# Kernel optimization log

Hardware: AMD Instinct MI355X
Metric: run time of the kernel (lower is better)

The kernel has to match this reference:

```python
import jax, jax.numpy as jnp
import numpy as np

VOCAB = 1500   # vocab_size
NE = 208       # n_embed
T = 256        # block_size
NH = 4         # n_head
HD = NE // NH  # head_size = 52
NL = 8         # n_layer
B = 256        # batch


def setup_inputs() -> dict:
    key = jax.random.key(0)
    ks = jax.random.split(key, 16)
    f = lambda k, shape: jax.random.normal(k, shape, jnp.float32) * 0.02
    return {
        "idx": jax.random.randint(ks[0], (B, T), 0, VOCAB),
        "targets": jax.random.randint(ks[1], (B, T), 0, VOCAB),
        "tok_emb": f(ks[2], (VOCAB, NE)),
        "pos_emb": f(ks[3], (T, NE)),
        # per-layer stacked attention params (separate no-bias Q/K/V Linears per head)
        "Wq": f(ks[4], (NL, NH, NE, HD)),
        "Wk": f(ks[5], (NL, NH, NE, HD)),
        "Wv": f(ks[6], (NL, NH, NE, HD)),
        "Wo": f(ks[7], (NL, NE, NE)),
        "bo": jnp.zeros((NL, NE), jnp.float32),
        "ln1_g": jnp.ones((NL, NE), jnp.float32),
        "ln1_b": jnp.zeros((NL, NE), jnp.float32),
        "W1": f(ks[8], (NL, NE, 4 * NE)),
        "b1": jnp.zeros((NL, 4 * NE), jnp.float32),
        "W2": f(ks[9], (NL, 4 * NE, NE)),
        "b2": jnp.zeros((NL, NE), jnp.float32),
        "ln2_g": jnp.ones((NL, NE), jnp.float32),
        "ln2_b": jnp.zeros((NL, NE), jnp.float32),
        "lnf_g": jnp.ones((NE,), jnp.float32),
        "lnf_b": jnp.zeros((NE,), jnp.float32),
        "Wlm": f(ks[10], (NE, VOCAB)),
        "blm": jnp.zeros((VOCAB,), jnp.float32),
    }


def _layernorm(x, g, b, eps=1e-5):
    mu = x.mean(-1, keepdims=True)
    var = ((x - mu) ** 2).mean(-1, keepdims=True)
    return (x - mu) * jax.lax.rsqrt(var + eps) * g + b


def reference(idx, targets, tok_emb, pos_emb, Wq, Wk, Wv, Wo, bo,
              ln1_g, ln1_b, W1, b1, W2, b2, ln2_g, ln2_b,
              lnf_g, lnf_b, Wlm, blm):
    x = tok_emb[idx] + pos_emb[None, :, :]          # [B, T, NE]
    mask = jnp.tril(jnp.ones((T, T), bool))
    scale = NE ** -0.5                               # NOTE: scales by n_embed, per source (C**-0.5)
    for i in range(NL):
        h = _layernorm(x, ln1_g[i], ln1_b[i])
        q = jnp.einsum('btc,hcd->bhtd', h, Wq[i])
        k = jnp.einsum('btc,hcd->bhtd', h, Wk[i])
        v = jnp.einsum('btc,hcd->bhtd', h, Wv[i])
        s = jnp.einsum('bhtd,bhsd->bhts', q, k) * scale
        s = jnp.where(mask, s, -jnp.inf)
        a = jax.nn.softmax(s, axis=-1)               # dropout is identity in eval
        o = jnp.einsum('bhts,bhsd->bhtd', a, v)
        o = o.transpose(0, 2, 1, 3).reshape(x.shape[0], T, NE)
        x = x + o @ Wo[i] + bo[i]
        h2 = _layernorm(x, ln2_g[i], ln2_b[i])
        x = x + jax.nn.relu(h2 @ W1[i] + b1[i]) @ W2[i] + b2[i]
    x = _layernorm(x, lnf_g, lnf_b)
    logits = (x @ Wlm + blm).reshape(-1, VOCAB)      # [B*T, VOCAB]
    logp = jax.nn.log_softmax(logits, axis=-1)
    loss = -jnp.take_along_axis(logp, targets.reshape(-1, 1), axis=-1).mean()
    return logits, loss
```

## Files before the change

kernel.cpp:

```cpp
#include <hip/hip_runtime.h>
#include <hip/hip_bf16.h>
#include <math.h>

#define VOCAB 1500
#define NE    208
#define TT    256
#define NHD   4
#define HD    52
#define NL    8
#define BBATCH 256
#define NTOK  (BBATCH * TT)
#define KP    224

typedef __attribute__((ext_vector_type(8))) short bf16x8;
typedef __attribute__((ext_vector_type(4))) short s16x4;
typedef __attribute__((ext_vector_type(4))) float f32x4;
typedef __attribute__((ext_vector_type(4))) int i32x4;
typedef __attribute__((ext_vector_type(4))) _Float16 f16x4;

__device__ __forceinline__ void gload16(const void* g, void* l) {
  __builtin_amdgcn_global_load_lds(
      (const __attribute__((address_space(1))) unsigned int*)g,
      (__attribute__((address_space(3))) unsigned int*)l, 16, 0, 0);
}
__device__ __forceinline__ float bf2f(short u) {
  union { unsigned int i; float f; } cv;
  cv.i = ((unsigned int)(unsigned short)u) << 16;
  return cv.f;
}
__device__ __forceinline__ short f2bf(float f) {
  return (short)__bfloat16_as_ushort(__float2bfloat16(f));
}

#define P_QKV 1146880
#define P_O   458752
#define P_1   1605632
#define P_2   1703936
#define P_LM  344064
__global__ __launch_bounds__(256) void k_prep_all(const float* __restrict__ Wq,
                                                  const float* __restrict__ Wk,
                                                  const float* __restrict__ Wv,
                                                  const float* __restrict__ Wo,
                                                  const float* __restrict__ W1,
                                                  const float* __restrict__ W2,
                                                  const float* __restrict__ Wlm,
                                                  __hip_bfloat16* __restrict__ qkvT,
                                                  __hip_bfloat16* __restrict__ oT,
                                                  __hip_bfloat16* __restrict__ t1,
                                                  __hip_bfloat16* __restrict__ t2,
                                                  __hip_bfloat16* __restrict__ lmT) {
  int gi = blockIdx.x * 256 + threadIdx.x;
  if (gi < P_QKV) {
    int i = gi;
    int c = i % KP;
    int jl = i / KP;
    int j = jl % 640, l = jl / 640;
    float v = 0.f;
    if (j < 624 && c < NE) {
      int sel = j / NE, hd = j - sel * NE;
      int h = hd / HD, d = hd - h * HD;
      const float* W = (sel == 0) ? Wq : (sel == 1) ? Wk : Wv;
      v = W[(((size_t)l * NHD + h) * NE + c) * HD + d];
    }
    qkvT[i] = __float2bfloat16(v);
  } else if (gi < P_QKV + P_O) {
    int i = gi - P_QKV;
    int c = i % KP;
    int jl = i / KP;
    int j = jl % 256, l = jl / 256;
    float v = (j < NE && c < NE) ? Wo[((size_t)l * NE + c) * NE + j] : 0.f;
    oT[i] = __float2bfloat16(v);
  } else if (gi < P_QKV + P_O + P_1) {
    int i = gi - (P_QKV + P_O);
    int c = i % KP;
    int jl = i / KP;
    int j = jl % 896, l = jl / 896;
    float v = (j < 832 && c < NE) ? W1[((size_t)l * NE + c) * 832 + j] : 0.f;
    t1[i] = __float2bfloat16(v);
  } else if (gi < P_QKV + P_O + P_1 + P_2) {
    int i = gi - (P_QKV + P_O + P_1);
    int c = i % 832;
    int jl = i / 832;
    int j = jl % 256, l = jl / 256;
    float v = (j < NE) ? W2[((size_t)l * 832 + c) * NE + j] : 0.f;
    t2[i] = __float2bfloat16(v);
  } else {
    int i = gi - (P_QKV + P_O + P_1 + P_2);
    int c = i % KP;
    int j = i / KP;
    float v = (j < VOCAB && c < NE) ? Wlm[(size_t)c * VOCAB + j] : 0.f;
    lmT[i] = __float2bfloat16(v);
  }
}

__global__ __launch_bounds__(256) void k_embed_ln(const int* __restrict__ idx,
                                                  const float* __restrict__ tok,
                                                  const float* __restrict__ pos,
                                                  const float* __restrict__ g,
                                                  const float* __restrict__ b,
                                                  __hip_bfloat16* __restrict__ x,
                                                  __hip_bfloat16* __restrict__ h) {
  int r = blockIdx.x * 4 + (threadIdx.x >> 6);
  int lane = threadIdx.x & 63;
  const int c0 = lane * 4;
  const int t = r & (TT - 1);
  float v[4] = {0.f, 0.f, 0.f, 0.f};
  float s = 0.f;
  if (lane < 52) {
    float4 tv = *(const float4*)(tok + (size_t)idx[r] * NE + c0);
    float4 pv = *(const float4*)(pos + (size_t)t * NE + c0);
    v[0] = tv.x + pv.x; v[1] = tv.y + pv.y;
    v[2] = tv.z + pv.z; v[3] = tv.w + pv.w;
    s = v[0] + v[1] + v[2] + v[3];
  }
  #pragma unroll
  for (int o = 32; o; o >>= 1) s += __shfl_xor(s, o);
  float mu = s * (1.f / NE);
  float q = 0.f;
  if (lane < 52) {
    #pragma unroll
    for (int i = 0; i < 4; i++) { float d = v[i] - mu; q += d * d; }
  }
  #pragma unroll
  for (int o = 32; o; o >>= 1) q += __shfl_xor(q, o);
  float inv = rsqrtf(q * (1.f / NE) + 1e-5f);
  if (lane < 52) {
    s16x4 xv;
    #pragma unroll
    for (int i = 0; i < 4; i++) xv[i] = f2bf(v[i]);
    *(s16x4*)(x + (size_t)r * NE + c0) = xv;
  }
  if (lane < 56) {
    s16x4 outv = {};
    if (lane < 52) {
      #pragma unroll
      for (int i = 0; i < 4; i++)
        outv[i] = f2bf((v[i] - mu) * inv * g[c0 + i] + b[c0 + i]);
    }
    *(s16x4*)(h + (size_t)r * KP + c0) = outv;
  }
}

template <bool RELU, bool BIAS, bool OUTBF, bool EXPSUM>
__global__ __launch_bounds__(256) void k_mgemm(const __hip_bfloat16* __restrict__ A, int lda,
                                               const __hip_bfloat16* __restrict__ BT, int ldb,
                                               const float* __restrict__ bias,
                                               void* __restrict__ Cout, int ldc,
                                               int N, int K,
                                               float* __restrict__ esum) {
  __shared__ __hip_bfloat16 As[2][128 * 32];
  __shared__ __hip_bfloat16 Bs[2][128 * 32];
  const int gx = gridDim.x;
  const int id = blockIdx.x + gx * blockIdx.y;
  const int qq = (gx * gridDim.y) >> 3;
  const int wid2 = (id & 7) * qq + (id >> 3);
  const int by = wid2 / gx, bx = wid2 - by * gx;
  const int bm = by * 128, bn = bx * 128;
  const int tid = threadIdx.x;
  const int wave = tid >> 6, lane = tid & 63;
  const int wr = (wave >> 1) * 64, wc = (wave & 1) * 64;
  const int l15 = lane & 15, l4 = lane >> 4;
  const int srow = tid >> 2, sgrp = (tid & 3) * 8;
  const int srow2 = srow + 64;
  f32x4 acc[4][4] = {};
  const int nt = K / 32;
  gload16(A + (size_t)(bm + srow) * lda + sgrp, &As[0][tid * 8]);
  gload16(BT + (size_t)(bn + srow) * ldb + sgrp, &Bs[0][tid * 8]);
  gload16(A + (size_t)(bm + srow2) * lda + sgrp, &As[0][(256 + tid) * 8]);
  gload16(BT + (size_t)(bn + srow2) * ldb + sgrp, &Bs[0][(256 + tid) * 8]);
  int cur = 0;
  for (int t = 0; t < nt; t++) {
    if (t + 1 < nt) {
      int k1 = (t + 1) * 32;
      gload16(A + (size_t)(bm + srow) * lda + k1 + sgrp, &As[cur ^ 1][tid * 8]);
      gload16(BT + (size_t)(bn + srow) * ldb + k1 + sgrp, &Bs[cur ^ 1][tid * 8]);
      gload16(A + (size_t)(bm + srow2) * lda + k1 + sgrp, &As[cur ^ 1][(256 + tid) * 8]);
      gload16(BT + (size_t)(bn + srow2) * ldb + k1 + sgrp, &Bs[cur ^ 1][(256 + tid) * 8]);
      asm volatile("s_waitcnt vmcnt(4)" ::: "memory");
    } else {
      asm volatile("s_waitcnt vmcnt(0)" ::: "memory");
    }
    __builtin_amdgcn_s_barrier();
    bf16x8 af[4], bfr[4];
    #pragma unroll
    for (int m = 0; m < 4; m++)
      af[m] = *(const bf16x8*)&As[cur][(wr + m * 16 + l15) * 32 + l4 * 8];
    #pragma unroll
    for (int n = 0; n < 4; n++)
      bfr[n] = *(const bf16x8*)&Bs[cur][(wc + n * 16 + l15) * 32 + l4 * 8];
    #pragma unroll
    for (int m = 0; m < 4; m++)
      #pragma unroll
      for (int n = 0; n < 4; n++)
        acc[m][n] = __builtin_amdgcn_mfma_f32_16x16x32_bf16(af[m], bfr[n], acc[m][n], 0, 0, 0);
    if (t + 1 < nt) __builtin_amdgcn_s_barrier();
    cur ^= 1;
  }
  float es[4][4];
  if (EXPSUM) {
    #pragma unroll
    for (int m = 0; m < 4; m++)
      #pragma unroll
      for (int j = 0; j < 4; j++) es[m][j] = 0.f;
  }
  #pragma unroll
  for (int m = 0; m < 4; m++) {
    #pragma unroll
    for (int n = 0; n < 4; n++) {
      int col = bn + wc + n * 16 + l15;
      if (col < N) {
        float bv = BIAS ? bias[col] : 0.f;
        #pragma unroll
        for (int j = 0; j < 4; j++) {
          int row = bm + wr + m * 16 + l4 * 4 + j;
          float v = acc[m][n][j] + bv;
          if (RELU) v = fmaxf(v, 0.f);
          size_t off = (size_t)row * ldc + col;
          if (OUTBF) ((__hip_bfloat16*)Cout)[off] = __float2bfloat16(v);
          else       ((float*)Cout)[off] = v;
          if (EXPSUM) es[m][j] += __expf(v);
        }
      }
    }
  }
  if (EXPSUM) {
    #pragma unroll
    for (int m = 0; m < 4; m++)
      #pragma unroll
      for (int j = 0; j < 4; j++) {
        float e = es[m][j];
        #pragma unroll
        for (int off = 1; off < 16; off <<= 1) e += __shfl_xor(e, off);
        if (l15 == 0) {
          int row = bm + wr + m * 16 + l4 * 4 + j;
          esum[(size_t)row * 24 + bx * 2 + (wave & 1)] = e;
        }
      }
  }
}

__global__ __launch_bounds__(512) void k_wo_mlp_ln(const __hip_bfloat16* __restrict__ hattn,
                                                   const __hip_bfloat16* __restrict__ WoT,
                                                   const float* __restrict__ bo,
                                                   const __hip_bfloat16* __restrict__ W1T,
                                                   const float* __restrict__ b1,
                                                   const __hip_bfloat16* __restrict__ W2T,
                                                   const float* __restrict__ b2,
                                                   const float* __restrict__ g2,
                                                   const float* __restrict__ bb2,
                                                   const float* __restrict__ gn,
                                                   const float* __restrict__ bn,
                                                   __hip_bfloat16* __restrict__ xio,
                                                   __hip_bfloat16* __restrict__ hout) {
  __shared__ __hip_bfloat16 Hs[128 * 232];
  __shared__ __hip_bfloat16 pool[39936];
  __hip_bfloat16 (*As)[128 * 32] = (__hip_bfloat16 (*)[128 * 32])pool;
  __hip_bfloat16 (*Bs)[256 * 32] = (__hip_bfloat16 (*)[256 * 32])(pool + 8192);
  __hip_bfloat16* W1s = pool;
  __hip_bfloat16* Ac  = pool + 14336;
  __hip_bfloat16 (*W2s)[256 * 32] = (__hip_bfloat16 (*)[256 * 32])(pool + 23552);
  __shared__ float sred[128][4], qred[128][4];
  const int bm = blockIdx.x * 128;
  const int tid = threadIdx.x;
  const int wid = tid >> 6, lane = tid & 63;
  const int l15 = lane & 15, l4 = lane >> 4;
  const int w2r = (wid >> 2) * 64, w2c = (wid & 3) * 64;
  const int w1r = (wid >> 1) * 32, w1c = (wid & 1) * 32;
  const int srow = tid >> 2, sgrp = (tid & 3) * 8;
  f32x4 xp[4][4] = {};
  {
    gload16(hattn + (size_t)(bm + srow) * KP + sgrp, &As[0][tid * 8]);
    gload16(WoT + (size_t)srow * KP + sgrp, &Bs[0][tid * 8]);
    gload16(WoT + (size_t)(128 + srow) * KP + sgrp, &Bs[0][(512 + tid) * 8]);
    int cur = 0;
    for (int t = 0; t < 7; t++) {
      if (t + 1 < 7) {
        int k1 = (t + 1) * 32;
        gload16(hattn + (size_t)(bm + srow) * KP + k1 + sgrp, &As[cur ^ 1][tid * 8]);
        gload16(WoT + (size_t)srow * KP + k1 + sgrp, &Bs[cur ^ 1][tid * 8]);
        gload16(WoT + (size_t)(128 + srow) * KP + k1 + sgrp, &Bs[cur ^ 1][(512 + tid) * 8]);
        asm volatile("s_waitcnt vmcnt(3)" ::: "memory");
      } else {
        asm volatile("s_waitcnt vmcnt(0)" ::: "memory");
      }
      __builtin_amdgcn_s_barrier();
      bf16x8 af[4], bfr[4];
      #pragma unroll
      for (int m = 0; m < 4; m++)
        af[m] = *(const bf16x8*)&As[cur][(w2r + m * 16 + l15) * 32 + l4 * 8];
      #pragma unroll
      for (int n = 0; n < 4; n++)
        bfr[n] = *(const bf16x8*)&Bs[cur][(w2c + n * 16 + l15) * 32 + l4 * 8];
      #pragma unroll
      for (int m = 0; m < 4; m++)
        #pragma unroll
        for (int n = 0; n < 4; n++)
          xp[m][n] = __builtin_amdgcn_mfma_f32_16x16x32_bf16(af[m], bfr[n], xp[m][n], 0, 0, 0);
      if (t + 1 < 7) __builtin_amdgcn_s_barrier();
      cur ^= 1;
    }
  }
  #pragma unroll
  for (int m = 0; m < 4; m++)
    #pragma unroll
    for (int j = 0; j < 4; j++) {
      int rowL = w2r + m * 16 + l4 * 4 + j;
      float s = 0.f, q = 0.f;
      #pragma unroll
      for (int n = 0; n < 4; n++) {
        int col = w2c + n * 16 + l15;
        float v = 0.f;
        if (col < NE)
          v = xp[m][n][j] + bo[col] +
              bf2f(((const short*)xio)[(size_t)(bm + rowL) * NE + col]);
        xp[m][n][j] = v;
        s += v; q += v * v;
      }
      #pragma unroll
      for (int off = 1; off < 16; off <<= 1) {
        s += __shfl_xor(s, off);
        q += __shfl_xor(q, off);
      }
      if (l15 == 0) { sred[rowL][wid & 3] = s; qred[rowL][wid & 3] = q; }
    }
  __syncthreads();
  #pragma unroll
  for (int m = 0; m < 4; m++)
    #pragma unroll
    for (int j = 0; j < 4; j++) {
      int rowL = w2r + m * 16 + l4 * 4 + j;
      float s = sred[rowL][0] + sred[rowL][1] + sred[rowL][2] + sred[rowL][3];
      float q = qred[rowL][0] + qred[rowL][1] + qred[rowL][2] + qred[rowL][3];
      float mu = s * (1.f / NE);
      float var = q * (1.f / NE) - mu * mu;
      float inv = rsqrtf(var + 1e-5f);
      #pragma unroll
      for (int n = 0; n < 4; n++) {
        int col = w2c + n * 16 + l15;
        if (col < NE)
          Hs[rowL * 232 + col] =
              __float2bfloat16((xp[m][n][j] - mu) * inv * g2[col] + bb2[col]);
      }
    }
  {
    int row = tid >> 2, c0 = 208 + (tid & 3) * 4;
    *(s16x4*)&Hs[row * 232 + c0] = (s16x4){};
  }
  __syncthreads();
  f32x4 acc2[4][4] = {};
  for (int jc = 0; jc < 13; jc++) {
    if (jc) __syncthreads();
    for (int s = tid; s < 1792; s += 512)
      gload16(W1T + (size_t)(jc * 64 + s / 28) * KP + (s % 28) * 8, &W1s[s * 8]);
    for (int s = tid; s < 2048; s += 512) {
      int kt2 = s >> 10, ss = s & 1023;
      gload16(W2T + (size_t)(ss >> 2) * 832 + jc * 64 + kt2 * 32 + (ss & 3) * 8,
              &W2s[kt2][ss * 8]);
    }
    __syncthreads();
    f32x4 acc1[2][2] = {};
    #pragma unroll
    for (int kt = 0; kt < 7; kt++) {
      bf16x8 a0 = *(const bf16x8*)&Hs[(w1r + l15) * 232 + kt * 32 + l4 * 8];
      bf16x8 a1 = *(const bf16x8*)&Hs[(w1r + 16 + l15) * 232 + kt * 32 + l4 * 8];
      bf16x8 c0 = *(const bf16x8*)&W1s[(w1c + l15) * 224 + kt * 32 + l4 * 8];
      bf16x8 c1 = *(const bf16x8*)&W1s[(w1c + 16 + l15) * 224 + kt * 32 + l4 * 8];
      acc1[0][0] = __builtin_amdgcn_mfma_f32_16x16x32_bf16(a0, c0, acc1[0][0], 0, 0, 0);
      acc1[0][1] = __builtin_amdgcn_mfma_f32_16x16x32_bf16(a0, c1, acc1[0][1], 0, 0, 0);
      acc1[1][0] = __builtin_amdgcn_mfma_f32_16x16x32_bf16(a1, c0, acc1[1][0], 0, 0, 0);
      acc1[1][1] = __builtin_amdgcn_mfma_f32_16x16x32_bf16(a1, c1, acc1[1][1], 0, 0, 0);
    }
    #pragma unroll
    for (int m = 0; m < 2; m++)
      #pragma unroll
      for (int n = 0; n < 2; n++) {
        int colL = w1c + n * 16 + l15;
        float bv = b1[jc * 64 + colL];
        #pragma unroll
        for (int j = 0; j < 4; j++) {
          int rowL = w1r + m * 16 + l4 * 4 + j;
          Ac[rowL * 72 + colL] = __float2bfloat16(fmaxf(acc1[m][n][j] + bv, 0.f));
        }
      }
    __syncthreads();
    #pragma unroll
    for (int kt2 = 0; kt2 < 2; kt2++) {
      bf16x8 af[4], bfr[4];
      #pragma unroll
      for (int m = 0; m < 4; m++)
        af[m] = *(const bf16x8*)&Ac[(w2r + m * 16 + l15) * 72 + kt2 * 32 + l4 * 8];
      #pragma unroll
      for (int n = 0; n < 4; n++)
        bfr[n] = *(const bf16x8*)&W2s[kt2][(w2c + n * 16 + l15) * 32 + l4 * 8];
      #pragma unroll
      for (int m = 0; m < 4; m++)
        #pragma unroll
        for (int n = 0; n < 4; n++)
          acc2[m][n] = __builtin_amdgcn_mfma_f32_16x16x32_bf16(af[m], bfr[n], acc2[m][n], 0, 0, 0);
    }
  }
  #pragma unroll
  for (int m2 = 0; m2 < 4; m2++)
    #pragma unroll
    for (int j = 0; j < 4; j++) {
      int rowL = w2r + m2 * 16 + l4 * 4 + j;
      float s = 0.f, q = 0.f;
      #pragma unroll
      for (int n2 = 0; n2 < 4; n2++) {
        int col = w2c + n2 * 16 + l15;
        float v = 0.f;
        if (col < NE) v = acc2[m2][n2][j] + b2[col] + xp[m2][n2][j];
        acc2[m2][n2][j] = v;
        s += v; q += v * v;
      }
      #pragma unroll
      for (int off = 1; off < 16; off <<= 1) {
        s += __shfl_xor(s, off);
        q += __shfl_xor(q, off);
      }
      if (l15 == 0) { sred[rowL][wid & 3] = s; qred[rowL][wid & 3] = q; }
    }
  __syncthreads();
  #pragma unroll
  for (int m2 = 0; m2 < 4; m2++)
    #pragma unroll
    for (int j = 0; j < 4; j++) {
      int rowL = w2r + m2 * 16 + l4 * 4 + j;
      float s = sred[rowL][0] + sred[rowL][1] + sred[rowL][2] + sred[rowL][3];
      float q = qred[rowL][0] + qred[rowL][1] + qred[rowL][2] + qred[rowL][3];
      float mu = s * (1.f / NE);
      float var = q * (1.f / NE) - mu * mu;
      float inv = rsqrtf(var + 1e-5f);
      size_t row = bm + rowL;
      #pragma unroll
      for (int n2 = 0; n2 < 4; n2++) {
        int col = w2c + n2 * 16 + l15;
        if (col < NE) {
          float v = acc2[m2][n2][j];
          xio[row * NE + col] = __float2bfloat16(v);
          hout[row * KP + col] = __float2bfloat16((v - mu) * inv * gn[col] + bn[col]);
        } else if (col < KP) {
          hout[row * KP + col] = __float2bfloat16(0.f);
        }
      }
    }
}

#define KSTRIDE 64
#define VSTRIDE 260
__global__ __launch_bounds__(256) void k_attn_mfma(const __hip_bfloat16* __restrict__ qkv,
                                                   __hip_bfloat16* __restrict__ o) {
  __shared__ __hip_bfloat16 Ks[256 * KSTRIDE];
  __shared__ _Float16      Vt[64 * VSTRIDE];
  const int bh0 = blockIdx.x;
  const int bh = (bh0 & 7) * 128 + (bh0 >> 3);
  const int b = bh >> 2, h = bh & 3;
  const __hip_bfloat16* base = qkv + (size_t)b * TT * 624;
  const int tid = threadIdx.x;
  #pragma unroll
  for (int it = 0; it < 16; it++) {
    int u = it * 256 + tid;
    int t = u >> 4, d4 = (u & 15) * 4;
    s16x4 v = {};
    if (d4 < 52) v = *(const s16x4*)(base + t * 624 + 208 + h * HD + d4);
    *(s16x4*)&Ks[t * KSTRIDE + d4] = v;
  }
  #pragma unroll
  for (int it = 0; it < 13; it++) {
    int slot = it * 256 + tid;
    int t = slot / 13, dl = (slot - t * 13) * 4;
    s16x4 kv = *(const s16x4*)(base + t * 624 + 416 + h * HD + dl);
    #pragma unroll
    for (int i = 0; i < 4; i++)
      Vt[(dl + i) * VSTRIDE + t] = (_Float16)bf2f(kv[i]);
  }
  #pragma unroll
  for (int it = 0; it < 12; it++)
    Vt[(52 + it) * VSTRIDE + tid] = (_Float16)0.f;
  __syncthreads();

  const int w = tid >> 6, lane = tid & 63, l15 = lane & 15, l4 = lane >> 4;
  const float scale = 0.06933752453f;
  const int qts[4] = {w, 7 - w, 8 + w, 15 - w};
  bf16x8 qf[4][2];
  #pragma unroll
  for (int i = 0; i < 4; i++) {
    const __hip_bfloat16* qrow = base + (qts[i] * 16 + l15) * 624 + h * HD;
    #pragma unroll
    for (int ks = 0; ks < 2; ks++) {
      int s = ks * 32 + l4 * 8;
      union { s16x4 h2[2]; bf16x8 v; } u;
      u.h2[0] = (s <= 48) ? *(const s16x4*)(qrow + s) : (s16x4){};
      u.h2[1] = (s <= 44) ? *(const s16x4*)(qrow + s + 4) : (s16x4){};
      qf[i][ks] = u.v;
    }
  }
  f32x4 oacc[4][4] = {};
  float mrun[4] = {-1e30f, -1e30f, -1e30f, -1e30f};
  float lrun[4] = {0.f, 0.f, 0.f, 0.f};
  const int cmax = 15 - w;
  for (int c = 0; c <= cmax; c++) {
    const int kb = c * 16;
    const bf16x8 kf0 = *(const bf16x8*)&Ks[(kb + l15) * KSTRIDE + l4 * 8];
    const bf16x8 kf1 = *(const bf16x8*)&Ks[(kb + l15) * KSTRIDE + 32 + l4 * 8];
    #pragma unroll
    for (int i = 0; i < 4; i++) {
      if (qts[i] < c) continue;
      __builtin_amdgcn_s_setprio(1);
      f32x4 s4 = __builtin_amdgcn_mfma_f32_16x16x32_bf16(kf0, qf[i][0],
                                                         (f32x4){0.f, 0.f, 0.f, 0.f}, 0, 0, 0);
      s4 = __builtin_amdgcn_mfma_f32_16x16x32_bf16(kf1, qf[i][1], s4, 0, 0, 0);
      __builtin_amdgcn_s_setprio(0);
      const int q = qts[i] * 16 + l15;
      float pv[4];
      float pmax = -1e30f;
      #pragma unroll
      for (int j = 0; j < 4; j++) {
        int key = kb + l4 * 4 + j;
        float s = s4[j] * scale;
        pv[j] = (key <= q) ? s : -1e30f;
        pmax = fmaxf(pmax, pv[j]);
      }
      pmax = fmaxf(pmax, __shfl_xor(pmax, 16));
      pmax = fmaxf(pmax, __shfl_xor(pmax, 32));
      if (!__all(pmax - mrun[i] <= 8.f)) {
        const float newm = fmaxf(mrun[i], pmax);
        const float r = __expf(mrun[i] - newm);
        lrun[i] *= r;
        mrun[i] = newm;
        #pragma unroll
        for (int m = 0; m < 4; m++) {
          oacc[m][i][0] *= r; oacc[m][i][1] *= r;
          oacc[m][i][2] *= r; oacc[m][i][3] *= r;
        }
      }
      float psum = 0.f;
      f16x4 pb;
      #pragma unroll
      for (int j = 0; j < 4; j++) {
        float e = __expf(pv[j] - mrun[i]);
        psum += e;
        pb[j] = (_Float16)e;
      }
      psum += __shfl_xor(psum, 16);
      psum += __shfl_xor(psum, 32);
      lrun[i] += psum;
      __builtin_amdgcn_s_setprio(1);
      #pragma unroll
      for (int m = 0; m < 4; m++) {
        f16x4 vf = *(const f16x4*)&Vt[(m * 16 + l15) * VSTRIDE + kb + l4 * 4];
        oacc[m][i] = __builtin_amdgcn_mfma_f32_16x16x16f16(vf, pb, oacc[m][i], 0, 0, 0);
      }
      __builtin_amdgcn_s_setprio(0);
    }
  }
  #pragma unroll
  for (int i = 0; i < 4; i++) {
    const float inv = 1.f / lrun[i];
    __hip_bfloat16* orow = o + (size_t)(b * TT + qts[i] * 16 + l15) * KP + h * HD;
    #pragma unroll
    for (int m = 0; m < 4; m++) {
      int d0 = m * 16 + l4 * 4;
      if (d0 + 3 < HD) {
        s16x4 pk;
        #pragma unroll
        for (int j = 0; j < 4; j++) pk[j] = f2bf(oacc[m][i][j] * inv);
        *(s16x4*)(orow + d0) = pk;
      }
    }
  }
}

__global__ __launch_bounds__(256) void k_loss_fin(const float* __restrict__ esum,
                                                  const float* __restrict__ logits,
                                                  const int* __restrict__ targets,
                                                  float* __restrict__ row_loss) {
  int r = blockIdx.x * 256 + threadIdx.x;
  const float* e = esum + (size_t)r * 24;
  float s = 0.f;
  #pragma unroll
  for (int i = 0; i < 24; i++) s += e[i];
  row_loss[r] = __logf(s) - logits[(size_t)r * VOCAB + targets[r]];
}

__global__ __launch_bounds__(256) void k_loss_reduce(const float* __restrict__ row_loss,
                                                     float* __restrict__ out_loss) {
  __shared__ float sh[256];
  float s = 0.f;
  for (int i = threadIdx.x; i < NTOK; i += 256) s += row_loss[i];
  sh[threadIdx.x] = s;
  __syncthreads();
  for (int k = 128; k; k >>= 1) {
    if (threadIdx.x < k) sh[threadIdx.x] += sh[threadIdx.x + k];
    __syncthreads();
  }
  if (threadIdx.x == 0) *out_loss = sh[0] * (1.f / NTOK);
}

extern "C" void kernel_launch(void* const* d_in, const int* in_sizes, int n_in,
                              void* d_out, int out_size, void* d_ws, size_t ws_size,
                              hipStream_t stream) {
  const int*   idx     = (const int*)d_in[0];
  const int*   targets = (const int*)d_in[1];
  const float* tok     = (const float*)d_in[2];
  const float* pos     = (const float*)d_in[3];
  const float* Wq      = (const float*)d_in[4];
  const float* Wk      = (const float*)d_in[5];
  const float* Wv      = (const float*)d_in[6];
  const float* Wo      = (const float*)d_in[7];
  const float* bo      = (const float*)d_in[8];
  const float* ln1g    = (const float*)d_in[9];
  const float* ln1b    = (const float*)d_in[10];
  const float* W1      = (const float*)d_in[11];
  const float* b1      = (const float*)d_in[12];
  const float* W2      = (const float*)d_in[13];
  const float* b2      = (const float*)d_in[14];
  const float* ln2g    = (const float*)d_in[15];
  const float* ln2b    = (const float*)d_in[16];
  const float* lnfg    = (const float*)d_in[17];
  const float* lnfb    = (const float*)d_in[18];
  const float* Wlm     = (const float*)d_in[19];
  const float* blm     = (const float*)d_in[20];
  float* out = (float*)d_out;

  char* w = (char*)d_ws;
  __hip_bfloat16* x   = (__hip_bfloat16*)w; w += (size_t)NTOK * NE * 2;
  __hip_bfloat16* qkv = (__hip_bfloat16*)w; w += (size_t)NTOK * 624 * 2;
  __hip_bfloat16* hbf = (__hip_bfloat16*)w; w += (size_t)NTOK * KP * 2;
  __hip_bfloat16* WqkvT = (__hip_bfloat16*)w; w += (size_t)P_QKV * 2;
  __hip_bfloat16* WoT   = (__hip_bfloat16*)w; w += (size_t)P_O * 2;
  __hip_bfloat16* W1T   = (__hip_bfloat16*)w; w += (size_t)P_1 * 2;
  __hip_bfloat16* W2T   = (__hip_bfloat16*)w; w += (size_t)P_2 * 2;
  __hip_bfloat16* WlmT  = (__hip_bfloat16*)w; w += (size_t)P_LM * 2;
  float* row_loss = (float*)w;              w += (size_t)NTOK * 4;
  float* esum     = (float*)w;

  k_prep_all<<<(P_QKV + P_O + P_1 + P_2 + P_LM) / 256, 256, 0, stream>>>(
      Wq, Wk, Wv, Wo, W1, W2, Wlm, WqkvT, WoT, W1T, W2T, WlmT);
  k_embed_ln<<<NTOK / 4, 256, 0, stream>>>(idx, tok, pos, ln1g, ln1b, x, hbf);

  for (int l = 0; l < NL; l++) {
    k_mgemm<false, false, true, false><<<dim3(5, 512), 256, 0, stream>>>(
        hbf, KP, WqkvT + (size_t)l * 640 * KP, KP, nullptr, qkv, 624, 624, KP, nullptr);
    k_attn_mfma<<<BBATCH * NHD, 256, 0, stream>>>(qkv, hbf);
    const float* gnp = (l < NL - 1) ? (ln1g + (l + 1) * NE) : lnfg;
    const float* bnp = (l < NL - 1) ? (ln1b + (l + 1) * NE) : lnfb;
    k_wo_mlp_ln<<<512, 512, 0, stream>>>(
        hbf, WoT + (size_t)l * 256 * KP, bo + l * NE,
        W1T + (size_t)l * 896 * KP, b1 + l * 832,
        W2T + (size_t)l * 256 * 832, b2 + l * NE,
        ln2g + l * NE, ln2b + l * NE, gnp, bnp, x, hbf);
  }

  k_mgemm<false, true, false, true><<<dim3(12, 512), 256, 0, stream>>>(
      hbf, KP, WlmT, KP, blm, out, VOCAB, VOCAB, KP, esum);

  k_loss_fin<<<NTOK / 256, 256, 0, stream>>>(esum, out, targets, row_loss);
  k_loss_reduce<<<1, 256, 0, stream>>>(row_loss, out + ((size_t)out_size - 1));
}
```

Before: 2.296 ms.

## Fuse per-head QKV projection into attention kernel, dropping qkv buffer

Each attention block (one batch, one head) now computes its own Q/K/V projection with MFMA from the layernormed activations and a per-head repacked weight, writing straight into LDS, then runs causal flash-style attention with 512 threads. This removes the separate QKV GEMM launch and the global round-trip of the 624-wide qkv tensor. In exchange the weight layout is redone per head, a separate hattn buffer is needed because hbf is still being read, and the large LDS footprint may limit occupancy. The layernormed input is also reloaded by all four heads of a batch.

Result: faster. 2.115 ms (median of 2 runs) (-7.9%).

```diff
diff --git a/kernel.cpp b/kernel.cpp
--- a/kernel.cpp
+++ b/kernel.cpp
@@ -32,11 +32,11 @@
   return (short)__bfloat16_as_ushort(__float2bfloat16(f));
 }
 
-#define P_QKV 1146880
-#define P_O   458752
-#define P_1   1605632
-#define P_2   1703936
-#define P_LM  344064
+#define P_QKVH 1835008
+#define P_O    458752
+#define P_1    1605632
+#define P_2    1703936
+#define P_LM   344064
 __global__ __launch_bounds__(256) void k_prep_all(const float* __restrict__ Wq,
                                                   const float* __restrict__ Wk,
                                                   const float* __restrict__ Wv,
@@ -44,48 +44,48 @@
                                                   const float* __restrict__ W1,
                                                   const float* __restrict__ W2,
                                                   const float* __restrict__ Wlm,
-                                                  __hip_bfloat16* __restrict__ qkvT,
+                                                  __hip_bfloat16* __restrict__ qkvH,
                                                   __hip_bfloat16* __restrict__ oT,
                                                   __hip_bfloat16* __restrict__ t1,
                                                   __hip_bfloat16* __restrict__ t2,
                                                   __hip_bfloat16* __restrict__ lmT) {
   int gi = blockIdx.x * 256 + threadIdx.x;
-  if (gi < P_QKV) {
+  if (gi < P_QKVH) {
     int i = gi;
     int c = i % KP;
-    int jl = i / KP;
-    int j = jl % 640, l = jl / 640;
+    int rhl = i / KP;
+    int r = rhl % 256, hl = rhl / 256;
+    int h = hl % NHD, l = hl / NHD;
     float v = 0.f;
-    if (j < 624 && c < NE) {
-      int sel = j / NE, hd = j - sel * NE;
-      int h = hd / HD, d = hd - h * HD;
-      const float* W = (sel == 0) ? Wq : (sel == 1) ? Wk : Wv;
+    if (c < NE && r < 156) {
+      const float* W = (r < 52) ? Wq : (r < 104) ? Wk : Wv;
+      int d = (r < 52) ? r : (r < 104) ? r - 52 : r - 104;
       v = W[(((size_t)l * NHD + h) * NE + c) * HD + d];
     }
-    qkvT[i] = __float2bfloat16(v);
-  } else if (gi < P_QKV + P_O) {
-    int i = gi - P_QKV;
+    qkvH[i] = __float2bfloat16(v);
+  } else if (gi < P_QKVH + P_O) {
+    int i = gi - P_QKVH;
     int c = i % KP;
     int jl = i / KP;
     int j = jl % 256, l = jl / 256;
     float v = (j < NE && c < NE) ? Wo[((size_t)l * NE + c) * NE + j] : 0.f;
     oT[i] = __float2bfloat16(v);
-  } else if (gi < P_QKV + P_O + P_1) {
-    int i = gi - (P_QKV + P_O);
+  } else if (gi < P_QKVH + P_O + P_1) {
+    int i = gi - (P_QKVH + P_O);
     int c = i % KP;
     int jl = i / KP;
     int j = jl % 896, l = jl / 896;
     float v = (j < 832 && c < NE) ? W1[((size_t)l * NE + c) * 832 + j] : 0.f;
     t1[i] = __float2bfloat16(v);
-  } else if (gi < P_QKV + P_O + P_1 + P_2) {
-    int i = gi - (P_QKV + P_O + P_1);
+  } else if (gi < P_QKVH + P_O + P_1 + P_2) {
+    int i = gi - (P_QKVH + P_O + P_1);
     int c = i % 832;
     int jl = i / 832;
     int j = jl % 256, l = jl / 256;
     float v = (j < NE) ? W2[((size_t)l * 832 + c) * NE + j] : 0.f;
     t2[i] = __float2bfloat16(v);
   } else {
-    int i = gi - (P_QKV + P_O + P_1 + P_2);
+    int i = gi - (P_QKVH + P_O + P_1 + P_2);
     int c = i % KP;
     int j = i / KP;
     float v = (j < VOCAB && c < NE) ? Wlm[(size_t)c * VOCAB + j] : 0.f;
@@ -99,7 +99,8 @@
                                                   const float* __restrict__ g,
                                                   const float* __restrict__ b,
                                                   __hip_bfloat16* __restrict__ x,
-                                                  __hip_bfloat16* __restrict__ h) {
+                                                  __hip_bfloat16* __restrict__ h,
+                                                  __hip_bfloat16* __restrict__ hattn) {
   int r = blockIdx.x * 4 + (threadIdx.x >> 6);
   int lane = threadIdx.x & 63;
   const int c0 = lane * 4;
@@ -138,6 +139,8 @@
         outv[i] = f2bf((v[i] - mu) * inv * g[c0 + i] + b[c0 + i]);
     }
     *(s16x4*)(h + (size_t)r * KP + c0) = outv;
+    if (lane >= 52)
+      *(s16x4*)(hattn + (size_t)r * KP + c0) = (s16x4){};
   }
 }
 
@@ -236,6 +239,169 @@
           esum[(size_t)row * 24 + bx * 2 + (wave & 1)] = e;
         }
       }
+  }
+}
+
+__global__ __launch_bounds__(512) void k_qkv_attn(const __hip_bfloat16* __restrict__ hbf,
+                                                  const __hip_bfloat16* __restrict__ WqkvH,
+                                                  __hip_bfloat16* __restrict__ o) {
+  __shared__ __hip_bfloat16 As2[2][256 * 32];
+  __shared__ __hip_bfloat16 Bs2[2][256 * 32];
+  __shared__ __hip_bfloat16 Ks[256 * 64];
+  __shared__ _Float16      Vt[64 * 260];
+  __shared__ __hip_bfloat16 Qs[256 * 56];
+  const int bh0 = blockIdx.x;
+  const int bh = (bh0 & 7) * 128 + (bh0 >> 3);
+  const int b = bh >> 2, h = bh & 3;
+  const __hip_bfloat16* A = hbf + (size_t)b * TT * KP;
+  const __hip_bfloat16* B = WqkvH + (size_t)h * 256 * KP;
+  const int tid = threadIdx.x;
+  const int w = tid >> 6, lane = tid & 63, l15 = lane & 15, l4 = lane >> 4;
+  {
+    const int s0 = tid, s1 = tid + 512;
+    const int r0 = s0 >> 2, g0 = (s0 & 3) * 8;
+    const int r1 = s1 >> 2, g1 = (s1 & 3) * 8;
+    f32x4 acc[2][10] = {};
+    gload16(A + (size_t)r0 * KP + g0, &As2[0][s0 * 8]);
+    gload16(A + (size_t)r1 * KP + g1, &As2[0][s1 * 8]);
+    gload16(B + (size_t)r0 * KP + g0, &Bs2[0][s0 * 8]);
+    gload16(B + (size_t)r1 * KP + g1, &Bs2[0][s1 * 8]);
+    int cur = 0;
+    for (int t = 0; t < 7; t++) {
+      if (t < 6) {
+        int k1 = (t + 1) * 32;
+        gload16(A + (size_t)r0 * KP + k1 + g0, &As2[cur ^ 1][s0 * 8]);
+        gload16(A + (size_t)r1 * KP + k1 + g1, &As2[cur ^ 1][s1 * 8]);
+        gload16(B + (size_t)r0 * KP + k1 + g0, &Bs2[cur ^ 1][s0 * 8]);
+        gload16(B + (size_t)r1 * KP + k1 + g1, &Bs2[cur ^ 1][s1 * 8]);
+        asm volatile("s_waitcnt vmcnt(4)" ::: "memory");
+      } else {
+        asm volatile("s_waitcnt vmcnt(0)" ::: "memory");
+      }
+      __builtin_amdgcn_s_barrier();
+      bf16x8 af[2], bfr[10];
+      #pragma unroll
+      for (int m = 0; m < 2; m++)
+        af[m] = *(const bf16x8*)&As2[cur][(w * 32 + m * 16 + l15) * 32 + l4 * 8];
+      #pragma unroll
+      for (int n = 0; n < 10; n++)
+        bfr[n] = *(const bf16x8*)&Bs2[cur][(n * 16 + l15) * 32 + l4 * 8];
+      #pragma unroll
+      for (int m = 0; m < 2; m++)
+        #pragma unroll
+        for (int n = 0; n < 10; n++)
+          acc[m][n] = __builtin_amdgcn_mfma_f32_16x16x32_bf16(af[m], bfr[n], acc[m][n], 0, 0, 0);
+      if (t < 6) __builtin_amdgcn_s_barrier();
+      cur ^= 1;
+    }
+    #pragma unroll
+    for (int m = 0; m < 2; m++)
+      #pragma unroll
+      for (int n = 0; n < 10; n++) {
+        int col = n * 16 + l15;
+        #pragma unroll
+        for (int j = 0; j < 4; j++) {
+          int trow = w * 32 + m * 16 + l4 * 4 + j;
+          float v = acc[m][n][j];
+          if (col < 52)        Qs[trow * 56 + col] = __float2bfloat16(v);
+          else if (col < 104)  Ks[trow * 64 + (col - 52)] = __float2bfloat16(v);
+          else if (col < 156)  Vt[(col - 104) * 260 + trow] = (_Float16)v;
+        }
+      }
+  }
+  for (int i = tid; i < 768; i += 512) {
+    int row = i / 3, cc = 52 + (i % 3) * 4;
+    *(s16x4*)&Ks[row * 64 + cc] = (s16x4){};
+  }
+  for (int i = tid; i < 3072; i += 512)
+    Vt[(52 + i / 256) * 260 + (i & 255)] = (_Float16)0.f;
+  if (tid < 256)
+    *(s16x4*)&Qs[tid * 56 + 52] = (s16x4){};
+  __syncthreads();
+  const float scale = 0.06933752453f;
+  const int qts[2] = {w, 15 - w};
+  bf16x8 qf[2][2];
+  #pragma unroll
+  for (int i = 0; i < 2; i++)
+    #pragma unroll
+    for (int ks = 0; ks < 2; ks++) {
+      int s = ks * 32 + l4 * 8;
+      qf[i][ks] = (s <= 48) ? *(const bf16x8*)&Qs[(qts[i] * 16 + l15) * 56 + s]
+                            : (bf16x8){};
+    }
+  f32x4 oacc[4][2] = {};
+  float mrun[2] = {-1e30f, -1e30f};
+  float lrun[2] = {0.f, 0.f};
+  const int cmax = 15 - w;
+  for (int c = 0; c <= cmax; c++) {
+    const int kb = c * 16;
+    const bf16x8 kf0 = *(const bf16x8*)&Ks[(kb + l15) * 64 + l4 * 8];
+    const bf16x8 kf1 = *(const bf16x8*)&Ks[(kb + l15) * 64 + 32 + l4 * 8];
+    #pragma unroll
+    for (int i = 0; i < 2; i++) {
+      if (qts[i] < c) continue;
+      __builtin_amdgcn_s_setprio(1);
+      f32x4 s4 = __builtin_amdgcn_mfma_f32_16x16x32_bf16(kf0, qf[i][0],
+                                                         (f32x4){0.f, 0.f, 0.f, 0.f}, 0, 0, 0);
+      s4 = __builtin_amdgcn_mfma_f32_16x16x32_bf16(kf1, qf[i][1], s4, 0, 0, 0);
+      __builtin_amdgcn_s_setprio(0);
+      const int q = qts[i] * 16 + l15;
+      float pv[4];
+      float pmax = -1e30f;
+      #pragma unroll
+      for (int j = 0; j < 4; j++) {
+        int key = kb + l4 * 4 + j;
+        float s = s4[j] * scale;
+        pv[j] = (key <= q) ? s : -1e30f;
+        pmax = fmaxf(pmax, pv[j]);
+      }
+      pmax = fmaxf(pmax, __shfl_xor(pmax, 16));
+      pmax = fmaxf(pmax, __shfl_xor(pmax, 32));
+      if (!__all(pmax - mrun[i] <= 8.f)) {
+        const float newm = fmaxf(mrun[i], pmax);
+        const float r = __expf(mrun[i] - newm);
+        lrun[i] *= r;
+        mrun[i] = newm;
+        #pragma unroll
+        for (int m = 0; m < 4; m++) {
+          oacc[m][i][0] *= r; oacc[m][i][1] *= r;
+          oacc[m][i][2] *= r; oacc[m][i][3] *= r;
+        }
+      }
+      float psum = 0.f;
+      f16x4 pb;
+      #pragma unroll
+      for (int j = 0; j < 4; j++) {
+        float e = __expf(pv[j] - mrun[i]);
+        psum += e;
+        pb[j] = (_Float16)e;
+      }
+      psum += __shfl_xor(psum, 16);
+      psum += __shfl_xor(psum, 32);
+      lrun[i] += psum;
+      __builtin_amdgcn_s_setprio(1);
+      #pragma unroll
+      for (int m = 0; m < 4; m++) {
+        f16x4 vf = *(const f16x4*)&Vt[(m * 16 + l15) * 260 + kb + l4 * 4];
+        oacc[m][i] = __builtin_amdgcn_mfma_f32_16x16x16f16(vf, pb, oacc[m][i], 0, 0, 0);
+      }
+      __builtin_amdgcn_s_setprio(0);
+    }
+  }
+  #pragma unroll
+  for (int i = 0; i < 2; i++) {
+    const float inv = 1.f / lrun[i];
+    __hip_bfloat16* orow = o + (size_t)(b * TT + qts[i] * 16 + l15) * KP + h * HD;
+    #pragma unroll
+    for (int m = 0; m < 4; m++) {
+      int d0 = m * 16 + l4 * 4;
+      if (d0 + 3 < HD) {
+        s16x4 pk;
+        #pragma unroll
+        for (int j = 0; j < 4; j++) pk[j] = f2bf(oacc[m][i][j] * inv);
+        *(s16x4*)(orow + d0) = pk;
+      }
+    }
   }
 }
 
@@ -446,131 +612,6 @@
     }
 }
 
-#define KSTRIDE 64
-#define VSTRIDE 260
-__global__ __launch_bounds__(256) void k_attn_mfma(const __hip_bfloat16* __restrict__ qkv,
-                                                   __hip_bfloat16* __restrict__ o) {
-  __shared__ __hip_bfloat16 Ks[256 * KSTRIDE];
-  __shared__ _Float16      Vt[64 * VSTRIDE];
-  const int bh0 = blockIdx.x;
-  const int bh = (bh0 & 7) * 128 + (bh0 >> 3);
-  const int b = bh >> 2, h = bh & 3;
-  const __hip_bfloat16* base = qkv + (size_t)b * TT * 624;
-  const int tid = threadIdx.x;
-  #pragma unroll
-  for (int it = 0; it < 16; it++) {
-    int u = it * 256 + tid;
-    int t = u >> 4, d4 = (u & 15) * 4;
-    s16x4 v = {};
-    if (d4 < 52) v = *(const s16x4*)(base + t * 624 + 208 + h * HD + d4);
-    *(s16x4*)&Ks[t * KSTRIDE + d4] = v;
-  }
-  #pragma unroll
-  for (int it = 0; it < 13; it++) {
-    int slot = it * 256 + tid;
-    int t = slot / 13, dl = (slot - t * 13) * 4;
-    s16x4 kv = *(const s16x4*)(base + t * 624 + 416 + h * HD + dl);
-    #pragma unroll
-    for (int i = 0; i < 4; i++)
-      Vt[(dl + i) * VSTRIDE + t] = (_Float16)bf2f(kv[i]);
-  }
-  #pragma unroll
-  for (int it = 0; it < 12; it++)
-    Vt[(52 + it) * VSTRIDE + tid] = (_Float16)0.f;
-  __syncthreads();
-
-  const int w = tid >> 6, lane = tid & 63, l15 = lane & 15, l4 = lane >> 4;
-  const float scale = 0.06933752453f;
-  const int qts[4] = {w, 7 - w, 8 + w, 15 - w};
-  bf16x8 qf[4][2];
-  #pragma unroll
-  for (int i = 0; i < 4; i++) {
-    const __hip_bfloat16* qrow = base + (qts[i] * 16 + l15) * 624 + h * HD;
-    #pragma unroll
-    for (int ks = 0; ks < 2; ks++) {
-      int s = ks * 32 + l4 * 8;
-      union { s16x4 h2[2]; bf16x8 v; } u;
-      u.h2[0] = (s <= 48) ? *(const s16x4*)(qrow + s) : (s16x4){};
-      u.h2[1] = (s <= 44) ? *(const s16x4*)(qrow + s + 4) : (s16x4){};
-      qf[i][ks] = u.v;
-    }
-  }
-  f32x4 oacc[4][4] = {};
-  float mrun[4] = {-1e30f, -1e30f, -1e30f, -1e30f};
-  float lrun[4] = {0.f, 0.f, 0.f, 0.f};
-  const int cmax = 15 - w;
-  for (int c = 0; c <= cmax; c++) {
-    const int kb = c * 16;
-    const bf16x8 kf0 = *(const bf16x8*)&Ks[(kb + l15) * KSTRIDE + l4 * 8];
-    const bf16x8 kf1 = *(const bf16x8*)&Ks[(kb + l15) * KSTRIDE + 32 + l4 * 8];
-    #pragma unroll
-    for (int i = 0; i < 4; i++) {
-      if (qts[i] < c) continue;
-      __builtin_amdgcn_s_setprio(1);
-      f32x4 s4 = __builtin_amdgcn_mfma_f32_16x16x32_bf16(kf0, qf[i][0],
-                                                         (f32x4){0.f, 0.f, 0.f, 0.f}, 0, 0, 0);
-      s4 = __builtin_amdgcn_mfma_f32_16x16x32_bf16(kf1, qf[i][1], s4, 0, 0, 0);
-      __builtin_amdgcn_s_setprio(0);
-      const int q = qts[i] * 16 + l15;
-      float pv[4];
-      float pmax = -1e30f;
-      #pragma unroll
-      for (int j = 0; j < 4; j++) {
-        int key = kb + l4 * 4 + j;
-        float s = s4[j] * scale;
-        pv[j] = (key <= q) ? s : -1e30f;
-        pmax = fmaxf(pmax, pv[j]);
-      }
-      pmax = fmaxf(pmax, __shfl_xor(pmax, 16));
-      pmax = fmaxf(pmax, __shfl_xor(pmax, 32));
-      if (!__all(pmax - mrun[i] <= 8.f)) {
-        const float newm = fmaxf(mrun[i], pmax);
-        const float r = __expf(mrun[i] - newm);
-        lrun[i] *= r;
-        mrun[i] = newm;
-        #pragma unroll
-        for (int m = 0; m < 4; m++) {
-          oacc[m][i][0] *= r; oacc[m][i][1] *= r;
-          oacc[m][i][2] *= r; oacc[m][i][3] *= r;
-        }
-      }
-      float psum = 0.f;
-      f16x4 pb;
-      #pragma unroll
-      for (int j = 0; j < 4; j++) {
-        float e = __expf(pv[j] - mrun[i]);
-        psum += e;
-        pb[j] = (_Float16)e;
-      }
-      psum += __shfl_xor(psum, 16);
-      psum += __shfl_xor(psum, 32);
-      lrun[i] += psum;
-      __builtin_amdgcn_s_setprio(1);
-      #pragma unroll
-      for (int m = 0; m < 4; m++) {
-        f16x4 vf = *(const f16x4*)&Vt[(m * 16 + l15) * VSTRIDE + kb + l4 * 4];
-        oacc[m][i] = __builtin_amdgcn_mfma_f32_16x16x16f16(vf, pb, oacc[m][i], 0, 0, 0);
-      }
-      __builtin_amdgcn_s_setprio(0);
-    }
-  }
-  #pragma unroll
-  for (int i = 0; i < 4; i++) {
-    const float inv = 1.f / lrun[i];
-    __hip_bfloat16* orow = o + (size_t)(b * TT + qts[i] * 16 + l15) * KP + h * HD;
-    #pragma unroll
-    for (int m = 0; m < 4; m++) {
-      int d0 = m * 16 + l4 * 4;
-      if (d0 + 3 < HD) {
-        s16x4 pk;
-        #pragma unroll
-        for (int j = 0; j < 4; j++) pk[j] = f2bf(oacc[m][i][j] * inv);
-        *(s16x4*)(orow + d0) = pk;
-      }
-    }
-  }
-}
-
 __global__ __launch_bounds__(256) void k_loss_fin(const float* __restrict__ esum,
                                                   const float* __restrict__ logits,
                                                   const int* __restrict__ targets,
@@ -624,10 +665,10 @@
   float* out = (float*)d_out;
 
   char* w = (char*)d_ws;
-  __hip_bfloat16* x   = (__hip_bfloat16*)w; w += (size_t)NTOK * NE * 2;
-  __hip_bfloat16* qkv = (__hip_bfloat16*)w; w += (size_t)NTOK * 624 * 2;
-  __hip_bfloat16* hbf = (__hip_bfloat16*)w; w += (size_t)NTOK * KP * 2;
-  __hip_bfloat16* WqkvT = (__hip_bfloat16*)w; w += (size_t)P_QKV * 2;
+  __hip_bfloat16* x     = (__hip_bfloat16*)w; w += (size_t)NTOK * NE * 2;
+  __hip_bfloat16* hbf   = (__hip_bfloat16*)w; w += (size_t)NTOK * KP * 2;
+  __hip_bfloat16* hattn = (__hip_bfloat16*)w; w += (size_t)NTOK * KP * 2;
+  __hip_bfloat16* WqkvH = (__hip_bfloat16*)w; w += (size_t)P_QKVH * 2;
   __hip_bfloat16* WoT   = (__hip_bfloat16*)w; w += (size_t)P_O * 2;
   __hip_bfloat16* W1T   = (__hip_bfloat16*)w; w += (size_t)P_1 * 2;
   __hip_bfloat16* W2T   = (__hip_bfloat16*)w; w += (size_t)P_2 * 2;
@@ -635,18 +676,17 @@
   float* row_loss = (float*)w;              w += (size_t)NTOK * 4;
   float* esum     = (float*)w;
 
-  k_prep_all<<<(P_QKV + P_O + P_1 + P_2 + P_LM) / 256, 256, 0, stream>>>(
-      Wq, Wk, Wv, Wo, W1, W2, Wlm, WqkvT, WoT, W1T, W2T, WlmT);
-  k_embed_ln<<<NTOK / 4, 256, 0, stream>>>(idx, tok, pos, ln1g, ln1b, x, hbf);
+  k_prep_all<<<(P_QKVH + P_O + P_1 + P_2 + P_LM) / 256, 256, 0, stream>>>(
+      Wq, Wk, Wv, Wo, W1, W2, Wlm, WqkvH, WoT, W1T, W2T, WlmT);
+  k_embed_ln<<<NTOK / 4, 256, 0, stream>>>(idx, tok, pos, ln1g, ln1b, x, hbf, hattn);
 
   for (int l = 0; l < NL; l++) {
-    k_mgemm<false, false, true, false><<<dim3(5, 512), 256, 0, stream>>>(
-        hbf, KP, WqkvT + (size_t)l * 640 * KP, KP, nullptr, qkv, 624, 624, KP, nullptr);
-    k_attn_mfma<<<BBATCH * NHD, 256, 0, stream>>>(qkv, hbf);
+    k_qkv_attn<<<BBATCH * NHD, 512, 0, stream>>>(
+        hbf, WqkvH + (size_t)l * NHD * 256 * KP, hattn);
     const float* gnp = (l < NL - 1) ? (ln1g + (l + 1) * NE) : lnfg;
     const float* bnp = (l < NL - 1) ? (ln1b + (l + 1) * NE) : lnfb;
     k_wo_mlp_ln<<<512, 512, 0, stream>>>(
-        hbf, WoT + (size_t)l * 256 * KP, bo + l * NE,
+        hattn, WoT + (size_t)l * 256 * KP, bo + l * NE,
         W1T + (size_t)l * 896 * KP, b1 + l * 832,
         W2T + (size_t)l * 256 * 832, b2 + l * NE,
         ln2g + l * NE, ln2b + l * NE, gnp, bnp, x, hbf);
```
